# Kernel optimization log

Hardware: AMD Instinct MI355X
Metric: run time of the kernel (lower is better)

The kernel has to match this reference:

```python
import jax, jax.numpy as jnp
import numpy as np

KS = 2            # kernel_size
NUM_SHARED = 3    # len(num_shared_channels)
NBR_PARAM = 3     # nbr_param_layers
COUT = 128        # num_shared_channels[-1] == num_inputs
NUM_INPUTS = 128
D_R = 320         # ts2vec_output_dims
GEN_LEN = NBR_PARAM * COUT * COUT * KS


def _causal_conv(x, w, b, d):
    # x: [N, Ci, T], w: [Co, Ci, K], b: [Co]; left-pad (K-1)*d == pad+chomp in torch
    N, Ci, T = x.shape
    K = w.shape[-1]
    pad = (K - 1) * d
    xp = jnp.pad(x, ((0, 0), (0, 0), (pad, 0)))
    out = jnp.zeros((N, w.shape[0], T), dtype=x.dtype)
    for k in range(K):  # K==2, tiny static loop
        out = out + jnp.einsum('oc,nct->not', w[:, :, k], xp[:, :, k * d:k * d + T])
    return out + b[None, :, None]


def _causal_conv_group(x, w, d):
    # groups=N conv with per-sample weights. x: [N, C, T], w: [N, Co, C, K], no bias
    N, C, T = x.shape
    K = w.shape[-1]
    pad = (K - 1) * d
    xp = jnp.pad(x, ((0, 0), (0, 0), (pad, 0)))
    out = jnp.zeros((N, w.shape[1], T), dtype=x.dtype)
    for k in range(K):
        out = out + jnp.einsum('noc,nct->not', w[..., k], xp[:, :, k * d:k * d + T])
    return out


def setup_inputs() -> dict:
    key = jax.random.key(0)
    ks = jax.random.split(key, 12)
    N, T = 16, 1024
    x = jax.random.normal(ks[0], (N, T, NUM_INPUTS), dtype=jnp.float32)
    r = jax.random.normal(ks[1], (N, D_R), dtype=jnp.float32)
    # shared TemporalBlock params (in==out==COUT, so no downsample conv)
    wscale = 1.0 / np.sqrt(COUT * KS)
    shared_w1 = wscale * jax.random.normal(ks[2], (NUM_SHARED, COUT, COUT, KS), dtype=jnp.float32)
    shared_b1 = 0.01 * jax.random.normal(ks[3], (NUM_SHARED, COUT), dtype=jnp.float32)
    shared_w2 = wscale * jax.random.normal(ks[4], (NUM_SHARED, COUT, COUT, KS), dtype=jnp.float32)
    shared_b2 = 0.01 * jax.random.normal(ks[5], (NUM_SHARED, COUT), dtype=jnp.float32)
    # hypernetwork (f_param_generator) + additive base weights (last_conv_layers)
    fparam_W = 0.01 * jax.random.normal(ks[6], (GEN_LEN, D_R), dtype=jnp.float32)
    fparam_b = 0.01 * jax.random.normal(ks[7], (GEN_LEN,), dtype=jnp.float32)
    last_bias = 0.001 * jax.random.normal(ks[8], (GEN_LEN,), dtype=jnp.float32) + 1.0 / (KS * COUT)
    # output head
    lin_W = (1.0 / np.sqrt(COUT)) * jax.random.normal(ks[9], (NUM_INPUTS, COUT), dtype=jnp.float32)
    lin_b = 0.01 * jax.random.normal(ks[10], (NUM_INPUTS,), dtype=jnp.float32)
    return {"x": x, "r": r, "f_out_same_in_size": 1,
            "shared_w1": shared_w1, "shared_b1": shared_b1,
            "shared_w2": shared_w2, "shared_b2": shared_b2,
            "fparam_W": fparam_W, "fparam_b": fparam_b, "last_bias": last_bias,
            "lin_W": lin_W, "lin_b": lin_b}


def reference(x, r, f_out_same_in_size, shared_w1, shared_b1, shared_w2, shared_b2,
              fparam_W, fparam_b, last_bias, lin_W, lin_b):
    N, T, _ = x.shape
    h = jnp.swapaxes(x, 1, 2)  # [N, C, T]
    # shared TemporalBlocks (dropout p=0 -> identity)
    for i in range(NUM_SHARED):
        d = 2 ** i
        res = h
        a = jax.nn.relu(_causal_conv(h, shared_w1[i], shared_b1[i], d))
        a = jax.nn.relu(_causal_conv(a, shared_w2[i], shared_b2[i], d))
        h = jax.nn.relu(a + res)
    # hypernet-generated per-sample grouped conv layers
    gen = r @ fparam_W.T + fparam_b + last_bias           # [N, GEN_LEN]
    allw = gen.reshape(NBR_PARAM, N, COUT, COUT, KS)      # same layout as torch .view
    for i in range(NBR_PARAM):
        d = 2 ** (NUM_SHARED + i)
        res = h
        c = _causal_conv_group(h, allw[i], d)
        h = jax.nn.relu(jax.nn.relu(c) + res)             # relu(dropout(relu(c)) + res), p=0
    out = jnp.einsum('nct,oc->nto', h, lin_W) + lin_b     # [N, T, NUM_INPUTS]
    if not f_out_same_in_size:
        out = out[:, -1, :]
    return out
```

## Files before the change

kernel.cpp:

```cpp
#include <hip/hip_runtime.h>

#define NB    16
#define TLEN  1024
#define CCH   128
#define DR    320

typedef _Float16 h8 __attribute__((ext_vector_type(8)));
typedef _Float16 h4 __attribute__((ext_vector_type(4)));
typedef _Float16 h2 __attribute__((ext_vector_type(2)));
typedef float    f4 __attribute__((ext_vector_type(4)));

__device__ __forceinline__ void gload16h(const _Float16* g, _Float16* l) {
  __builtin_amdgcn_global_load_lds(
      (const __attribute__((address_space(1))) void*)g,
      (__attribute__((address_space(3))) void*)l, 16, 0, 0);
}
__device__ __forceinline__ void gload16f(const float* g, float* l) {
  __builtin_amdgcn_global_load_lds(
      (const __attribute__((address_space(1))) void*)g,
      (__attribute__((address_space(3))) void*)l, 16, 0, 0);
}

__global__ __launch_bounds__(256) void k_init(const float* __restrict__ w1,
                                              const float* __restrict__ w2,
                                              const float* __restrict__ linw,
                                              _Float16* __restrict__ Wsh,
                                              _Float16* __restrict__ linWh) {
  int i = blockIdx.x * 256 + threadIdx.x;
  {
    int c = i & 127, k = (i >> 7) & 1, o = (i >> 8) & 127, i3 = i >> 15;
    const float* srcw = (i3 < 3) ? (w1 + i3 * 32768) : (w2 + (i3 - 3) * 32768);
    Wsh[i] = (_Float16)srcw[(o * 128 + c) * 2 + k];
  }
  if (i < 16384) linWh[i] = (_Float16)linw[i];
}

struct SGen {
  float buf[3][32 * DR];
  float csc[4][16][16];
  float fbl[384];
  float lbl[384];
};
struct SPair {
  _Float16 hin[84 * 128];
  _Float16 a[80 * 128];
};
union alignas(16) SU { SGen g; SPair p; };

__device__ __forceinline__ void gen_body(SGen& S, int bid, int tid,
                                         const float* __restrict__ r,
                                         const float* __restrict__ fW,
                                         const float* __restrict__ fb,
                                         const float* __restrict__ lb,
                                         _Float16* __restrict__ wg) {
  constexpr int NT = 12;
  const size_t rbase = (size_t)bid * 384;

  const int l = tid & 63, w = tid >> 6;
  const int l15 = l & 15, lh = l >> 4;
  const int rt = w >> 1, kh = w & 1;

  f4 rx[5], ry[5];
  const float* rp = r + l15 * DR + kh * 160 + lh * 8;
#pragma unroll
  for (int cb = 0; cb < 5; cb++) {
    rx[cb] = *(const f4*)(rp + cb * 32);
    ry[cb] = *(const f4*)(rp + cb * 32 + 4);
  }
  if (tid < 96) {
    gload16f(fb + rbase + tid * 4, S.fbl + tid * 4);
    gload16f(lb + rbase + tid * 4, S.lbl + tid * 4);
  }
#pragma unroll
  for (int t = 0; t < 3; t++) {
    const float* s = fW + (rbase + (size_t)t * 32) * DR;
#pragma unroll
    for (int i = 0; i < 10; i++) {
      int f = tid + i * 256;
      gload16f(s + (size_t)f * 4, (float*)S.buf[t] + (size_t)f * 4);
    }
  }
  h8 bfr[5];
#pragma unroll
  for (int cb = 0; cb < 5; cb++) {
    h8 v;
    v[0] = (_Float16)rx[cb][0]; v[1] = (_Float16)rx[cb][1];
    v[2] = (_Float16)rx[cb][2]; v[3] = (_Float16)rx[cb][3];
    v[4] = (_Float16)ry[cb][0]; v[5] = (_Float16)ry[cb][1];
    v[6] = (_Float16)ry[cb][2]; v[7] = (_Float16)ry[cb][3];
    bfr[cb] = v;
  }
  asm volatile("s_waitcnt vmcnt(20) lgkmcnt(0)" ::: "memory");
  __builtin_amdgcn_s_barrier();
  __builtin_amdgcn_sched_barrier(0);

  const int rn = tid >> 4, rk = (tid >> 3) & 1, rcq = tid & 7;

  for (int j = 0; j < NT; j++) {
    const float* bp = (const float*)S.buf[j % 3];
    f4 acc = {0.f, 0.f, 0.f, 0.f};
    const float* arow = bp + (rt * 16 + l15) * DR + kh * 160 + lh * 8;
#pragma unroll
    for (int cb = 0; cb < 5; cb++) {
      f4 x = *(const f4*)(arow + cb * 32);
      f4 y = *(const f4*)(arow + cb * 32 + 4);
      h8 a;
      a[0] = (_Float16)x[0]; a[1] = (_Float16)x[1];
      a[2] = (_Float16)x[2]; a[3] = (_Float16)x[3];
      a[4] = (_Float16)y[0]; a[5] = (_Float16)y[1];
      a[6] = (_Float16)y[2]; a[7] = (_Float16)y[3];
      acc = __builtin_amdgcn_mfma_f32_16x16x32_f16(a, bfr[cb], acc, 0, 0, 0);
    }
#pragma unroll
    for (int rr = 0; rr < 4; rr++) S.csc[w][lh * 4 + rr][l15] = acc[rr];

    asm volatile("s_waitcnt lgkmcnt(0)" ::: "memory");
    __builtin_amdgcn_s_barrier();
    __builtin_amdgcn_sched_barrier(0);

    {
      const unsigned g32 = (unsigned)(rbase + (size_t)j * 32);
      const unsigned G = g32 >> 15, o = (g32 >> 8) & 127u, c0 = (g32 & 255u) >> 1;
      h2 v2;
#pragma unroll
      for (int i = 0; i < 2; i++) {
        int rl32 = (rcq * 2 + i) * 2 + rk;
        int hp = (rl32 >> 4) * 2, rr2 = rl32 & 15;
        float s = S.csc[hp][rr2][rn] + S.csc[hp + 1][rr2][rn] +
                  S.fbl[j * 32 + rl32] + S.lbl[j * 32 + rl32];
        v2[i] = (_Float16)s;
      }
      unsigned q = 3u * (unsigned)rn + G;
      *(h2*)&wg[(((size_t)q * 128 + o) * 2 + rk) * 128 + c0 + rcq * 2] = v2;
    }
    __builtin_amdgcn_sched_barrier(0);

    if (j + 3 < NT) {
      float* dstb = (float*)S.buf[j % 3];
      const float* src = fW + (rbase + (size_t)(j + 3) * 32) * DR;
#pragma unroll
      for (int i = 0; i < 10; i++) {
        int f = tid + i * 256;
        gload16f(src + (size_t)f * 4, dstb + (size_t)f * 4);
      }
    }

    if (j == 0)
      asm volatile("s_waitcnt vmcnt(21) lgkmcnt(0)" ::: "memory");
    else if (j + 4 <= NT)
      asm volatile("s_waitcnt vmcnt(22) lgkmcnt(0)" ::: "memory");
    else if (j + 3 == NT)
      asm volatile("s_waitcnt vmcnt(12) lgkmcnt(0)" ::: "memory");
    else
      asm volatile("s_waitcnt vmcnt(0) lgkmcnt(0)" ::: "memory");
    __builtin_amdgcn_s_barrier();
    __builtin_amdgcn_sched_barrier(0);
  }
}

template <int D>
__device__ __forceinline__ void pair_body(SPair& S, int tx, int n, int tid,
                                          const float* xin, _Float16* out,
                                          const _Float16* w1p, const _Float16* w2p,
                                          const float* b1p, const float* b2p) {
  constexpr int HA = 16;
  constexpr int HI = HA + D;
  constexpr int RIN = 80 + D;
  static_assert(RIN * 128 <= sizeof(SPair::hin) / sizeof(_Float16), "hin size");
  _Float16* hin_l = S.hin;
  _Float16* a_l = S.a;
  const int t0 = tx * 64;
  const float* xN = xin + (size_t)n * (TLEN * CCH);

  const int flo = (tx == 0) ? HI * 16 : 0;
  if (tx == 0) {
    for (int f = tid; f < HI * 16; f += 256)
      *(int4*)(hin_l + (size_t)f * 8) = make_int4(0, 0, 0, 0);
  }
  for (int f = flo + tid; f < RIN * 16; f += 256) {
    int p = f >> 4, l16 = f & 15;
    int c8 = (l16 ^ (p & 15)) << 3;
    const float* sp = xN + (size_t)(t0 - HI + p) * 128 + c8;
    f4 xa = *(const f4*)sp, xb = *(const f4*)(sp + 4);
    h8 v;
    v[0] = (_Float16)xa[0]; v[1] = (_Float16)xa[1];
    v[2] = (_Float16)xa[2]; v[3] = (_Float16)xa[3];
    v[4] = (_Float16)xb[0]; v[5] = (_Float16)xb[1];
    v[6] = (_Float16)xb[2]; v[7] = (_Float16)xb[3];
    *(h8*)(hin_l + (size_t)f * 8) = v;
  }
  __syncthreads();

  const int l = tid & 63, w = tid >> 6;
  const int l15 = l & 15, lh = l >> 4;
  const int o0 = w * 32;

  f4 acc1[2][5] = {};
#pragma unroll
  for (int tap = 0; tap < 2; tap++) {
#pragma unroll
    for (int cb = 0; cb < 4; cb++) {
      const int c0 = cb * 32 + lh * 8;
      h8 a[2], bfr[5];
#pragma unroll
      for (int i2 = 0; i2 < 2; i2++) {
        int o = o0 + i2 * 16 + l15;
        a[i2] = *(const h8*)&w1p[(o * 2 + tap) * 128 + c0];
      }
#pragma unroll
      for (int jt = 0; jt < 5; jt++) {
        int p = jt * 16 + l15 + tap * D;
        int cs = c0 ^ ((p & 15) << 3);
        bfr[jt] = *(const h8*)&hin_l[p * 128 + cs];
      }
#pragma unroll
      for (int i2 = 0; i2 < 2; i2++)
#pragma unroll
        for (int jt = 0; jt < 5; jt++)
          acc1[i2][jt] = __builtin_amdgcn_mfma_f32_16x16x32_f16(
              a[i2], bfr[jt], acc1[i2][jt], 0, 0, 0);
    }
  }
#pragma unroll
  for (int i2 = 0; i2 < 2; i2++) {
    f4 bv = *(const f4*)&b1p[o0 + i2 * 16 + lh * 4];
    const int base8 = o0 + i2 * 16 + (lh >> 1) * 8;
    const int sub = (lh & 1) * 4;
#pragma unroll
    for (int jt = 0; jt < 5; jt++) {
      int p = jt * 16 + l15;
      h4 sv;
      if (tx == 0 && jt == 0) {
        sv[0] = sv[1] = sv[2] = sv[3] = (_Float16)0.f;
      } else {
        f4 v = acc1[i2][jt];
#pragma unroll
        for (int rr = 0; rr < 4; rr++) sv[rr] = (_Float16)fmaxf(v[rr] + bv[rr], 0.f);
      }
      *(h4*)&a_l[p * 128 + (base8 ^ ((p & 15) << 3)) + sub] = sv;
    }
  }
  __syncthreads();

  f4 acc2[2][4] = {};
#pragma unroll
  for (int tap = 0; tap < 2; tap++) {
#pragma unroll
    for (int cb = 0; cb < 4; cb++) {
      const int c0 = cb * 32 + lh * 8;
      h8 a[2], bfr[4];
#pragma unroll
      for (int i2 = 0; i2 < 2; i2++) {
        int o = o0 + i2 * 16 + l15;
        a[i2] = *(const h8*)&w2p[(o * 2 + tap) * 128 + c0];
      }
#pragma unroll
      for (int jt = 0; jt < 4; jt++) {
        int pa = jt * 16 + l15 + (HA - D) + tap * D;
        int cs = c0 ^ ((pa & 15) << 3);
        bfr[jt] = *(const h8*)&a_l[pa * 128 + cs];
      }
#pragma unroll
      for (int i2 = 0; i2 < 2; i2++)
#pragma unroll
        for (int jt = 0; jt < 4; jt++)
          acc2[i2][jt] = __builtin_amdgcn_mfma_f32_16x16x32_f16(
              a[i2], bfr[jt], acc2[i2][jt], 0, 0, 0);
    }
  }

  _Float16* outN = out + (size_t)n * (TLEN * CCH);
#pragma unroll
  for (int i2 = 0; i2 < 2; i2++) {
    f4 bv = *(const f4*)&b2p[o0 + i2 * 16 + lh * 4];
    const int base8 = o0 + i2 * 16 + (lh >> 1) * 8;
    const int sub = (lh & 1) * 4;
#pragma unroll
    for (int jt = 0; jt < 4; jt++) {
      int t = t0 + jt * 16 + l15;
      int pr = jt * 16 + l15 + HA + D;
      h4 rv = *(const h4*)&hin_l[pr * 128 + (base8 ^ ((pr & 15) << 3)) + sub];
      f4 v = acc2[i2][jt];
      h4 sv;
#pragma unroll
      for (int rr = 0; rr < 4; rr++) {
        float z = fmaxf(v[rr] + bv[rr], 0.f);
        sv[rr] = (_Float16)fmaxf(z + (float)rv[rr], 0.f);
      }
      *(h4*)&outN[t * 128 + o0 + i2 * 16 + lh * 4] = sv;
    }
  }
}

__global__ __launch_bounds__(256, 1) void k_genpair(
    const float* __restrict__ r, const float* __restrict__ fW,
    const float* __restrict__ fb, const float* __restrict__ lb,
    _Float16* __restrict__ wg,
    const float* __restrict__ x, _Float16* __restrict__ h1,
    const _Float16* __restrict__ Wsh,
    const float* __restrict__ b1, const float* __restrict__ b2) {
  __shared__ SU su;
  const int bid = blockIdx.x, tid = threadIdx.x;
  gen_body(su.g, bid, tid, r, fW, fb, lb, wg);
  __syncthreads();
  pair_body<1>(su.p, bid & 15, bid >> 4, tid, x, h1,
               Wsh, Wsh + 3 * 32768, b1, b2);
}

template <int D, int NJ, bool GOUT>
__device__ __forceinline__ void pstage(const _Float16* __restrict__ w1p,
                                       const _Float16* __restrict__ w2p,
                                       const float* __restrict__ b1p,
                                       const float* __restrict__ b2p,
                                       const _Float16* __restrict__ inb,
                                       _Float16* __restrict__ ab,
                                       _Float16* __restrict__ outb,
                                       _Float16* __restrict__ goutN, int t0,
                                       int zlimA, int zlimO, int tid) {
  constexpr int NA = NJ + 1;
  const int l = tid & 63, w = tid >> 6;
  const int l15 = l & 15, lh = l >> 4;
  const int o0 = w * 32;
  const int base8 = o0 + (lh >> 1) * 8;
  const int sub = (lh & 1) * 4;

  f4 acc1[2][NA] = {};
#pragma unroll
  for (int tap = 0; tap < 2; tap++) {
#pragma unroll
    for (int cb = 0; cb < 4; cb++) {
      const int c0 = cb * 32 + lh * 8;
      h8 a[2], bfr[NA];
#pragma unroll
      for (int i2 = 0; i2 < 2; i2++) {
        int o = o0 + i2 * 16 + l15;
        a[i2] = *(const h8*)&w1p[(o * 2 + tap) * 128 + c0];
      }
#pragma unroll
      for (int jt = 0; jt < NA; jt++) {
        int p = jt * 16 + l15 + tap * D;
        int cs = c0 ^ ((p & 15) << 3);
        bfr[jt] = *(const h8*)&inb[p * 128 + cs];
      }
#pragma unroll
      for (int i2 = 0; i2 < 2; i2++)
#pragma unroll
        for (int jt = 0; jt < NA; jt++)
          acc1[i2][jt] = __builtin_amdgcn_mfma_f32_16x16x32_f16(
              a[i2], bfr[jt], acc1[i2][jt], 0, 0, 0);
    }
  }
#pragma unroll
  for (int i2 = 0; i2 < 2; i2++) {
    f4 bv = *(const f4*)&b1p[o0 + i2 * 16 + lh * 4];
    const int b8 = base8 + i2 * 16;
#pragma unroll
    for (int jt = 0; jt < NA; jt++) {
      int q = jt * 16 + l15;
      h4 sv;
      if (q < zlimA) {
        sv[0] = sv[1] = sv[2] = sv[3] = (_Float16)0.f;
      } else {
        f4 v = acc1[i2][jt];
#pragma unroll
        for (int rr = 0; rr < 4; rr++) sv[rr] = (_Float16)fmaxf(v[rr] + bv[rr], 0.f);
      }
      *(h4*)&ab[q * 128 + (b8 ^ ((q & 15) << 3)) + sub] = sv;
    }
  }
  __syncthreads();

  f4 acc2[2][NJ] = {};
#pragma unroll
  for (int tap = 0; tap < 2; tap++) {
#pragma unroll
    for (int cb = 0; cb < 4; cb++) {
      const int c0 = cb * 32 + lh * 8;
      h8 a[2], bfr[NJ];
#pragma unroll
      for (int i2 = 0; i2 < 2; i2++) {
        int o = o0 + i2 * 16 + l15;
        a[i2] = *(const h8*)&w2p[(o * 2 + tap) * 128 + c0];
      }
#pragma unroll
      for (int jt = 0; jt < NJ; jt++) {
        int pa = jt * 16 + l15 + (16 - 2 * D) + tap * D;
        int cs = c0 ^ ((pa & 15) << 3);
        bfr[jt] = *(const h8*)&ab[pa * 128 + cs];
      }
#pragma unroll
      for (int i2 = 0; i2 < 2; i2++)
#pragma unroll
        for (int jt = 0; jt < NJ; jt++)
          acc2[i2][jt] = __builtin_amdgcn_mfma_f32_16x16x32_f16(
              a[i2], bfr[jt], acc2[i2][jt], 0, 0, 0);
    }
  }
#pragma unroll
  for (int i2 = 0; i2 < 2; i2++) {
    f4 bv = *(const f4*)&b2p[o0 + i2 * 16 + lh * 4];
    const int b8 = base8 + i2 * 16;
#pragma unroll
    for (int jt = 0; jt < NJ; jt++) {
      int r = jt * 16 + l15;
      int pr = r + 16;
      h4 sv;
      if (r < zlimO) {
        sv[0] = sv[1] = sv[2] = sv[3] = (_Float16)0.f;
      } else {
        h4 rv = *(const h4*)&inb[pr * 128 + (b8 ^ ((pr & 15) << 3)) + sub];
        f4 v = acc2[i2][jt];
#pragma unroll
        for (int rr = 0; rr < 4; rr++) {
          float z = fmaxf(v[rr] + bv[rr], 0.f);
          sv[rr] = (_Float16)fmaxf(z + (float)rv[rr], 0.f);
        }
      }
      if (GOUT) {
        int t = t0 + r;
        *(h4*)&goutN[t * 128 + o0 + i2 * 16 + lh * 4] = sv;
      } else {
        *(h4*)&outb[r * 128 + (b8 ^ (l15 << 3)) + sub] = sv;
      }
    }
  }
}

__global__ __launch_bounds__(256) void k_pair24(const _Float16* __restrict__ in,
                                                _Float16* __restrict__ out,
                                                const _Float16* __restrict__ Wsh,
                                                const float* __restrict__ b1,
                                                const float* __restrict__ b2) {
  __shared__ _Float16 B0[104 * 128];
  __shared__ _Float16 B1[96 * 128];
  __shared__ _Float16 B2[88 * 128];
  const int tid = threadIdx.x;
  const int tx = blockIdx.x, n = blockIdx.y;
  const int t0 = tx * 64;
  const _Float16* inN = in + (size_t)n * (TLEN * CCH);

  for (int f = 96 * 16 + tid; f < 104 * 16; f += 256)
    *(int4*)(B0 + (size_t)f * 8) = make_int4(0, 0, 0, 0);
  for (int f = 80 * 16 + tid; f < 88 * 16; f += 256)
    *(int4*)(B2 + (size_t)f * 8) = make_int4(0, 0, 0, 0);

  if (tx == 0) {
    for (int f = tid; f < 32 * 16; f += 256)
      *(int4*)(B0 + (size_t)f * 8) = make_int4(0, 0, 0, 0);
    for (int f = 32 * 16 + tid; f < 96 * 16; f += 256) {
      int p = f >> 4, l16 = f & 15;
      int c8 = (l16 ^ (p & 15)) << 3;
      gload16h(inN + (t0 - 32 + p) * 128 + c8, B0 + f * 8);
    }
  } else {
    for (int f = tid; f < 96 * 16; f += 256) {
      int p = f >> 4, l16 = f & 15;
      int c8 = (l16 ^ (p & 15)) << 3;
      gload16h(inN + (t0 - 32 + p) * 128 + c8, B0 + f * 8);
    }
  }
  __syncthreads();

  pstage<2, 5, false>(Wsh + 1 * 32768, Wsh + 4 * 32768, b1 + 128, b2 + 128,
                      B0, B1, B2, nullptr, t0,
                      (tx == 0) ? 30 : 0, (tx == 0) ? 16 : 0, tid);
  __syncthreads();
  pstage<4, 4, true>(Wsh + 2 * 32768, Wsh + 5 * 32768, b1 + 256, b2 + 256,
                     B2, B1, nullptr,
                     out + (size_t)n * (TLEN * CCH), t0,
                     (tx == 0) ? 12 : 0, 0, tid);
}

template <int D, int NJ>
__device__ __forceinline__ void gstage(const _Float16* __restrict__ Wl,
                                       const _Float16* __restrict__ inb,
                                       _Float16* __restrict__ outb,
                                       int zlim, int tid) {
  const int l = tid & 63, w = tid >> 6;
  const int l15 = l & 15, lh = l >> 4;
  const int o0 = w * 32;
  f4 acc[2][NJ] = {};

#pragma unroll
  for (int tap = 0; tap < 2; tap++) {
#pragma unroll
    for (int cb = 0; cb < 4; cb++) {
      const int c0 = cb * 32 + 8 * lh;
      h8 a[2], bfr[NJ];
#pragma unroll
      for (int i2 = 0; i2 < 2; i2++) {
        int o = o0 + i2 * 16 + l15;
        int cs = c0 ^ ((o & 15) << 3);
        a[i2] = *(const h8*)&Wl[(o * 2 + tap) * 128 + cs];
      }
#pragma unroll
      for (int jt = 0; jt < NJ; jt++) {
        int p = jt * 16 + l15 + tap * D;
        int cs = c0 ^ ((p & 15) << 3);
        bfr[jt] = *(const h8*)&inb[p * 128 + cs];
      }
#pragma unroll
      for (int i2 = 0; i2 < 2; i2++)
#pragma unroll
        for (int jt = 0; jt < NJ; jt++)
          acc[i2][jt] = __builtin_amdgcn_mfma_f32_16x16x32_f16(
              a[i2], bfr[jt], acc[i2][jt], 0, 0, 0);
    }
  }

#pragma unroll
  for (int i2 = 0; i2 < 2; i2++) {
    const int base8 = o0 + i2 * 16 + (lh >> 1) * 8;
    const int sub = (lh & 1) * 4;
#pragma unroll
    for (int jt = 0; jt < NJ; jt++) {
      int rrow = jt * 16 + l15;
      int pr = rrow + D;
      h4 sv;
      if (rrow < zlim) {
        sv[0] = sv[1] = sv[2] = sv[3] = (_Float16)0.f;
      } else {
        h4 rv = *(const h4*)&inb[pr * 128 + (base8 ^ ((pr & 15) << 3)) + sub];
        f4 v = acc[i2][jt];
#pragma unroll
        for (int rr = 0; rr < 4; rr++) {
          float z = fmaxf(v[rr], 0.f);
          sv[rr] = (_Float16)fmaxf(z + (float)rv[rr], 0.f);
        }
      }
      *(h4*)&outb[rrow * 128 + (base8 ^ (l15 << 3)) + sub] = sv;
    }
  }
}

__global__ __launch_bounds__(256, 1) void k_group(const _Float16* __restrict__ in,
                                                  float* __restrict__ outp,
                                                  const _Float16* __restrict__ wg,
                                                  const _Float16* __restrict__ linWh,
                                                  const float* __restrict__ lbias) {
  __shared__ _Float16 bufA[120 * 128];
  __shared__ _Float16 bufB[112 * 128];
  __shared__ _Float16 Wl[256 * 128];
  const int tid = threadIdx.x;
  const int bid = blockIdx.x;
  const int n = (bid & 7) | (((bid >> 3) & 1) << 3);
  const int tx = bid >> 4;
  const int t0 = tx * 64;
  const _Float16* inN = in + (size_t)n * (TLEN * CCH);
  const _Float16* wp1 = wg + (size_t)n * 32768;
  const _Float16* wp2 = wg + 524288 + (size_t)n * 32768;
  const _Float16* wp3 = wg + 1048576 + (size_t)n * 32768;

  if (tx == 0) {
    for (int f = tid; f < 56 * 16; f += 256)
      *(int4*)(bufA + (size_t)f * 8) = make_int4(0, 0, 0, 0);
    for (int f = 56 * 16 + tid; f < 120 * 16; f += 256) {
      int p = f >> 4, l16 = f & 15;
      int c8 = (l16 ^ (p & 15)) << 3;
      gload16h(inN + (t0 - 56 + p) * 128 + c8, bufA + f * 8);
    }
  } else {
    for (int f = tid; f < 120 * 16; f += 256) {
      int p = f >> 4, l16 = f & 15;
      int c8 = (l16 ^ (p & 15)) << 3;
      gload16h(inN + (t0 - 56 + p) * 128 + c8, bufA + f * 8);
    }
  }
  for (int f = tid; f < 4096; f += 256) {
    int row = f >> 4, l16 = f & 15;
    int c8 = (l16 ^ ((row >> 1) & 15)) << 3;
    gload16h(wp1 + row * 128 + c8, Wl + f * 8);
  }
  __syncthreads();

  gstage<8, 7>(Wl, bufA, bufB, (tx == 0) ? 48 : 0, tid);
  __syncthreads();
  for (int f = tid; f < 4096; f += 256) {
    int row = f >> 4, l16 = f & 15;
    int c8 = (l16 ^ ((row >> 1) & 15)) << 3;
    gload16h(wp2 + row * 128 + c8, Wl + f * 8);
  }
  __syncthreads();

  gstage<16, 6>(Wl, bufB, bufA, (tx == 0) ? 32 : 0, tid);
  __syncthreads();
  for (int f = tid; f < 4096; f += 256) {
    int row = f >> 4, l16 = f & 15;
    int c8 = (l16 ^ ((row >> 1) & 15)) << 3;
    gload16h(wp3 + row * 128 + c8, Wl + f * 8);
  }
  __syncthreads();

  gstage<32, 4>(Wl, bufA, bufB, 0, tid);
  __syncthreads();

  const int l = tid & 63, w = tid >> 6;
  const int l15 = l & 15, lh = l >> 4;
  const int o0 = w * 32;
  f4 acc3[2][4] = {};
#pragma unroll
  for (int cb = 0; cb < 4; cb++) {
    const int c0 = cb * 32 + lh * 8;
    h8 a[2], bfr[4];
#pragma unroll
    for (int i2 = 0; i2 < 2; i2++) {
      int o = o0 + i2 * 16 + l15;
      a[i2] = *(const h8*)&linWh[o * 128 + c0];
    }
#pragma unroll
    for (int jt = 0; jt < 4; jt++) {
      int p = jt * 16 + l15;
      int cs = c0 ^ ((p & 15) << 3);
      bfr[jt] = *(const h8*)&bufB[p * 128 + cs];
    }
#pragma unroll
    for (int i2 = 0; i2 < 2; i2++)
#pragma unroll
      for (int jt = 0; jt < 4; jt++)
        acc3[i2][jt] = __builtin_amdgcn_mfma_f32_16x16x32_f16(
            a[i2], bfr[jt], acc3[i2][jt], 0, 0, 0);
  }

#pragma unroll
  for (int i2 = 0; i2 < 2; i2++) {
    int o = o0 + i2 * 16 + lh * 4;
    f4 bv = *(const f4*)&lbias[o];
#pragma unroll
    for (int jt = 0; jt < 4; jt++) {
      int t = t0 + jt * 16 + l15;
      f4 v = acc3[i2][jt];
      float4 sv = make_float4(v[0] + bv[0], v[1] + bv[1], v[2] + bv[2], v[3] + bv[3]);
      *(float4*)&outp[((size_t)n * TLEN + t) * CCH + o] = sv;
    }
  }
}

extern "C" void kernel_launch(void* const* d_in, const int* in_sizes, int n_in,
                              void* d_out, int out_size, void* d_ws, size_t ws_size,
                              hipStream_t stream) {
  const float* x  = (const float*)d_in[0];
  const float* r  = (const float*)d_in[1];
  const float* w1 = (const float*)d_in[3];
  const float* b1 = (const float*)d_in[4];
  const float* w2 = (const float*)d_in[5];
  const float* b2 = (const float*)d_in[6];
  const float* fW = (const float*)d_in[7];
  const float* fb = (const float*)d_in[8];
  const float* lb = (const float*)d_in[9];
  const float* lw = (const float*)d_in[10];
  const float* lbias = (const float*)d_in[11];
  float* out = (float*)d_out;

  _Float16* h0    = (_Float16*)d_ws;
  _Float16* h1    = h0 + 2097152;
  _Float16* Wsh   = h1 + 2097152;
  _Float16* linWh = Wsh + 393216;
  _Float16* Wg    = linWh + 16384;

  k_init<<<768, 256, 0, stream>>>(w1, w2, lw, Wsh, linWh);
  k_genpair<<<256, 256, 0, stream>>>(r, fW, fb, lb, Wg, x, h1, Wsh, b1, b2);
  k_pair24<<<dim3(16, 16), 256, 0, stream>>>(h1, h0, Wsh, b1, b2);
  k_group<<<256, 256, 0, stream>>>(h0, out, Wg, linWh, lbias);
}
```

Measured before the change: 68.93 us.

## Fuse shared blocks 2-3 with grouped conv layers into single tail kernel

Merges the k_pair24 and k_group kernels into one k_tail kernel. Each block computes shared TemporalBlocks 2 and 3 over an enlarged halo (96 rows of history), then runs the three hypernet grouped convs and the linear head entirely in LDS. Grouped weights are now read straight from global memory instead of being staged into LDS. This removes a kernel launch and the fp16 intermediate round trip through global memory, at the cost of recomputing halo rows and using more LDS per block.

Measured after the change: 70.11 us. About the same (+1.7%).

```diff
diff --git a/kernel.cpp b/kernel.cpp
--- a/kernel.cpp
+++ b/kernel.cpp
@@ -166,7 +166,6 @@
   constexpr int HA = 16;
   constexpr int HI = HA + D;
   constexpr int RIN = 80 + D;
-  static_assert(RIN * 128 <= sizeof(SPair::hin) / sizeof(_Float16), "hin size");
   _Float16* hin_l = S.hin;
   _Float16* a_l = S.a;
   const int t0 = tx * 64;
@@ -426,56 +425,11 @@
   }
 }
 
-__global__ __launch_bounds__(256) void k_pair24(const _Float16* __restrict__ in,
-                                                _Float16* __restrict__ out,
-                                                const _Float16* __restrict__ Wsh,
-                                                const float* __restrict__ b1,
-                                                const float* __restrict__ b2) {
-  __shared__ _Float16 B0[104 * 128];
-  __shared__ _Float16 B1[96 * 128];
-  __shared__ _Float16 B2[88 * 128];
-  const int tid = threadIdx.x;
-  const int tx = blockIdx.x, n = blockIdx.y;
-  const int t0 = tx * 64;
-  const _Float16* inN = in + (size_t)n * (TLEN * CCH);
-
-  for (int f = 96 * 16 + tid; f < 104 * 16; f += 256)
-    *(int4*)(B0 + (size_t)f * 8) = make_int4(0, 0, 0, 0);
-  for (int f = 80 * 16 + tid; f < 88 * 16; f += 256)
-    *(int4*)(B2 + (size_t)f * 8) = make_int4(0, 0, 0, 0);
-
-  if (tx == 0) {
-    for (int f = tid; f < 32 * 16; f += 256)
-      *(int4*)(B0 + (size_t)f * 8) = make_int4(0, 0, 0, 0);
-    for (int f = 32 * 16 + tid; f < 96 * 16; f += 256) {
-      int p = f >> 4, l16 = f & 15;
-      int c8 = (l16 ^ (p & 15)) << 3;
-      gload16h(inN + (t0 - 32 + p) * 128 + c8, B0 + f * 8);
-    }
-  } else {
-    for (int f = tid; f < 96 * 16; f += 256) {
-      int p = f >> 4, l16 = f & 15;
-      int c8 = (l16 ^ (p & 15)) << 3;
-      gload16h(inN + (t0 - 32 + p) * 128 + c8, B0 + f * 8);
-    }
-  }
-  __syncthreads();
-
-  pstage<2, 5, false>(Wsh + 1 * 32768, Wsh + 4 * 32768, b1 + 128, b2 + 128,
-                      B0, B1, B2, nullptr, t0,
-                      (tx == 0) ? 30 : 0, (tx == 0) ? 16 : 0, tid);
-  __syncthreads();
-  pstage<4, 4, true>(Wsh + 2 * 32768, Wsh + 5 * 32768, b1 + 256, b2 + 256,
-                     B2, B1, nullptr,
-                     out + (size_t)n * (TLEN * CCH), t0,
-                     (tx == 0) ? 12 : 0, 0, tid);
-}
-
-template <int D, int NJ>
-__device__ __forceinline__ void gstage(const _Float16* __restrict__ Wl,
-                                       const _Float16* __restrict__ inb,
-                                       _Float16* __restrict__ outb,
-                                       int zlim, int tid) {
+template <int D, int NJ, int XR>
+__device__ __forceinline__ void gstage_g(const _Float16* __restrict__ wp,
+                                         const _Float16* __restrict__ inb,
+                                         _Float16* __restrict__ outb,
+                                         int zlim, int tid) {
   const int l = tid & 63, w = tid >> 6;
   const int l15 = l & 15, lh = l >> 4;
   const int o0 = w * 32;
@@ -490,13 +444,12 @@
 #pragma unroll
       for (int i2 = 0; i2 < 2; i2++) {
         int o = o0 + i2 * 16 + l15;
-        int cs = c0 ^ ((o & 15) << 3);
-        a[i2] = *(const h8*)&Wl[(o * 2 + tap) * 128 + cs];
+        a[i2] = *(const h8*)&wp[(o * 2 + tap) * 128 + c0];
       }
 #pragma unroll
       for (int jt = 0; jt < NJ; jt++) {
         int p = jt * 16 + l15 + tap * D;
-        int cs = c0 ^ ((p & 15) << 3);
+        int cs = (c0 ^ ((p & 15) << 3)) ^ XR;
         bfr[jt] = *(const h8*)&inb[p * 128 + cs];
       }
 #pragma unroll
@@ -520,7 +473,7 @@
       if (rrow < zlim) {
         sv[0] = sv[1] = sv[2] = sv[3] = (_Float16)0.f;
       } else {
-        h4 rv = *(const h4*)&inb[pr * 128 + (base8 ^ ((pr & 15) << 3)) + sub];
+        h4 rv = *(const h4*)&inb[pr * 128 + ((base8 ^ ((pr & 15) << 3)) ^ XR) + sub];
         f4 v = acc[i2][jt];
 #pragma unroll
         for (int rr = 0; rr < 4; rr++) {
@@ -533,14 +486,17 @@
   }
 }
 
-__global__ __launch_bounds__(256, 1) void k_group(const _Float16* __restrict__ in,
-                                                  float* __restrict__ outp,
-                                                  const _Float16* __restrict__ wg,
-                                                  const _Float16* __restrict__ linWh,
-                                                  const float* __restrict__ lbias) {
-  __shared__ _Float16 bufA[120 * 128];
-  __shared__ _Float16 bufB[112 * 128];
-  __shared__ _Float16 Wl[256 * 128];
+__global__ __launch_bounds__(256, 1) void k_tail(const _Float16* __restrict__ in,
+                                                 float* __restrict__ outp,
+                                                 const _Float16* __restrict__ Wsh,
+                                                 const float* __restrict__ b1,
+                                                 const float* __restrict__ b2,
+                                                 const _Float16* __restrict__ wg,
+                                                 const _Float16* __restrict__ linWh,
+                                                 const float* __restrict__ lbias) {
+  __shared__ _Float16 B0[164 * 128];
+  __shared__ _Float16 B1[160 * 128];
+  __shared__ _Float16 B2[152 * 128];
   const int tid = threadIdx.x;
   const int bid = blockIdx.x;
   const int n = (bid & 7) | (((bid >> 3) & 1) << 3);
@@ -551,47 +507,35 @@
   const _Float16* wp2 = wg + 524288 + (size_t)n * 32768;
   const _Float16* wp3 = wg + 1048576 + (size_t)n * 32768;
 
-  if (tx == 0) {
-    for (int f = tid; f < 56 * 16; f += 256)
-      *(int4*)(bufA + (size_t)f * 8) = make_int4(0, 0, 0, 0);
-    for (int f = 56 * 16 + tid; f < 120 * 16; f += 256) {
-      int p = f >> 4, l16 = f & 15;
-      int c8 = (l16 ^ (p & 15)) << 3;
-      gload16h(inN + (t0 - 56 + p) * 128 + c8, bufA + f * 8);
-    }
-  } else {
-    for (int f = tid; f < 120 * 16; f += 256) {
-      int p = f >> 4, l16 = f & 15;
-      int c8 = (l16 ^ (p & 15)) << 3;
-      gload16h(inN + (t0 - 56 + p) * 128 + c8, bufA + f * 8);
-    }
-  }
-  for (int f = tid; f < 4096; f += 256) {
-    int row = f >> 4, l16 = f & 15;
-    int c8 = (l16 ^ ((row >> 1) & 15)) << 3;
-    gload16h(wp1 + row * 128 + c8, Wl + f * 8);
-  }
-  __syncthreads();
-
-  gstage<8, 7>(Wl, bufA, bufB, (tx == 0) ? 48 : 0, tid);
-  __syncthreads();
-  for (int f = tid; f < 4096; f += 256) {
-    int row = f >> 4, l16 = f & 15;
-    int c8 = (l16 ^ ((row >> 1) & 15)) << 3;
-    gload16h(wp2 + row * 128 + c8, Wl + f * 8);
-  }
-  __syncthreads();
-
-  gstage<16, 6>(Wl, bufB, bufA, (tx == 0) ? 32 : 0, tid);
-  __syncthreads();
-  for (int f = tid; f < 4096; f += 256) {
-    int row = f >> 4, l16 = f & 15;
-    int c8 = (l16 ^ ((row >> 1) & 15)) << 3;
-    gload16h(wp3 + row * 128 + c8, Wl + f * 8);
-  }
-  __syncthreads();
-
-  gstage<32, 4>(Wl, bufA, bufB, 0, tid);
+  for (int f = 160 * 16 + tid; f < 164 * 16; f += 256)
+    *(int4*)(B0 + (size_t)f * 8) = make_int4(0, 0, 0, 0);
+  for (int f = 144 * 16 + tid; f < 152 * 16; f += 256)
+    *(int4*)(B2 + (size_t)f * 8) = make_int4(0, 0, 0, 0);
+
+  const int zr = (t0 < 96) ? (96 - t0) : 0;
+  for (int f = tid; f < zr * 16; f += 256)
+    *(int4*)(B0 + (size_t)f * 8) = make_int4(0, 0, 0, 0);
+  for (int f = zr * 16 + tid; f < 160 * 16; f += 256) {
+    int p = f >> 4, l16 = f & 15;
+    int c8 = (l16 ^ (p & 15)) << 3;
+    gload16h(inN + (size_t)(t0 - 96 + p) * 128 + c8, B0 + f * 8);
+  }
+  __syncthreads();
+
+  pstage<2, 9, false>(Wsh + 1 * 32768, Wsh + 4 * 32768, b1 + 128, b2 + 128,
+                      B0, B1, B2, nullptr, t0,
+                      (t0 < 94) ? (94 - t0) : 0, (t0 < 80) ? (80 - t0) : 0, tid);
+  __syncthreads();
+  pstage<4, 8, false>(Wsh + 2 * 32768, Wsh + 5 * 32768, b1 + 256, b2 + 256,
+                      B2, B1, B0, nullptr, t0,
+                      (t0 < 76) ? (76 - t0) : 0, (t0 < 64) ? (64 - t0) : 0, tid);
+  __syncthreads();
+
+  gstage_g<8, 7, 64>(wp1, B0 + 8 * 128, B2, (t0 < 48) ? (48 - t0) : 0, tid);
+  __syncthreads();
+  gstage_g<16, 6, 0>(wp2, B2, B1, (t0 < 32) ? (32 - t0) : 0, tid);
+  __syncthreads();
+  gstage_g<32, 4, 0>(wp3, B1, B2, 0, tid);
   __syncthreads();
 
   const int l = tid & 63, w = tid >> 6;
@@ -611,7 +555,7 @@
     for (int jt = 0; jt < 4; jt++) {
       int p = jt * 16 + l15;
       int cs = c0 ^ ((p & 15) << 3);
-      bfr[jt] = *(const h8*)&bufB[p * 128 + cs];
+      bfr[jt] = *(const h8*)&B2[p * 128 + cs];
     }
 #pragma unroll
     for (int i2 = 0; i2 < 2; i2++)
@@ -651,14 +595,12 @@
   const float* lbias = (const float*)d_in[11];
   float* out = (float*)d_out;
 
-  _Float16* h0    = (_Float16*)d_ws;
-  _Float16* h1    = h0 + 2097152;
+  _Float16* h1    = (_Float16*)d_ws;
   _Float16* Wsh   = h1 + 2097152;
   _Float16* linWh = Wsh + 393216;
   _Float16* Wg    = linWh + 16384;
 
   k_init<<<768, 256, 0, stream>>>(w1, w2, lw, Wsh, linWh);
   k_genpair<<<256, 256, 0, stream>>>(r, fW, fb, lb, Wg, x, h1, Wsh, b1, b2);
-  k_pair24<<<dim3(16, 16), 256, 0, stream>>>(h1, h0, Wsh, b1, b2);
-  k_group<<<256, 256, 0, stream>>>(h0, out, Wg, linWh, lbias);
-}
+  k_tail<<<256, 256, 0, stream>>>(h1, out, Wsh, b1, b2, Wg, linWh, lbias);
+}
```
